# Kernel tuning notes

Hardware: AMD Instinct MI355X
Metric: run time of the kernel (lower is better)

Reference implementation:

```python
import jax, jax.numpy as jnp
import numpy as np

B, T, C = 16, 2048, 384
HEAD = 384

def setup_inputs() -> dict:
    key = jax.random.key(0)
    kx, kq, kk, kv = jax.random.split(key, 4)
    s = 1.0 / np.sqrt(C)
    return {
        "x": jax.random.normal(kx, (B, T, C), dtype=jnp.float32),
        "Wq": jax.random.normal(kq, (C, HEAD), dtype=jnp.float32) * s,
        "Wk": jax.random.normal(kk, (C, HEAD), dtype=jnp.float32) * s,
        "Wv": jax.random.normal(kv, (C, HEAD), dtype=jnp.float32) * s,
    }

def reference(x, Wq, Wk, Wv):
    # x: [B,T,C]; single causal attention head, eval mode (dropout = identity)
    Bc, Tc, Cc = x.shape
    q = jnp.einsum('btc,ch->bth', x, Wq)
    k = jnp.einsum('btc,ch->bth', x, Wk)
    v = jnp.einsum('btc,ch->bth', x, Wv)
    # NOTE: original scales by C**-0.5 (embedding dim), not head_size**-0.5
    scale = Cc ** (-0.5)
    wei = jnp.einsum('bth,bsh->bts', q, k) * scale  # [B,T,T]
    causal = jnp.tril(jnp.ones((Tc, Tc), dtype=bool))
    wei = jnp.where(causal, wei, -jnp.inf)
    wei = jax.nn.softmax(wei, axis=-1)
    out = jnp.einsum('bts,bsh->bth', wei, v)  # [B,T,head]
    return out
```

## Files before the change

### kernel.cpp

```cpp
#include <hip/hip_runtime.h>
#include <hip/hip_bf16.h>

#define NB 16
#define TT 2048
#define CC 384

typedef short bf16x8 __attribute__((ext_vector_type(8)));
typedef float f32x4 __attribute__((ext_vector_type(4)));

static __device__ __forceinline__ short f2bf(float f) {
  union { __hip_bfloat16 h; short s; } u;
  u.h = __float2bfloat16(f);
  return u.s;
}

#define QSC (0.051031036307982884f * 1.4426950408889634f)

__global__ __launch_bounds__(384)
void conv_wt(const float* __restrict__ Wq, const float* __restrict__ Wk,
             const float* __restrict__ Wv, short* __restrict__ Wbt) {
  const int w = blockIdx.x / CC;
  const int n = blockIdx.x % CC;
  const int k = threadIdx.x;
  const float* W = (w == 0) ? Wq : (w == 1) ? Wk : Wv;
  Wbt[((size_t)w * CC + n) * CC + k] = f2bf(W[(size_t)k * CC + n]);
}

__global__ __launch_bounds__(256, 3)
void proj_gemm(const float* __restrict__ x, const short* __restrict__ Wbt,
               short* __restrict__ Q, short* __restrict__ K,
               short* __restrict__ Vt) {
  __shared__ char smem[34816];
  short* As = (short*)smem;
  short* Bs = (short*)(smem + 10240);
  short* Es = (short*)smem;

  const int mt = blockIdx.x & 255;
  const int nt = blockIdx.x >> 8;
  const int wsel = nt / 3;
  const int nc0 = (nt % 3) * 128;
  const int tid = threadIdx.x;
  const int wave = tid >> 6, lane = tid & 63;
  const int l15 = lane & 15, quad = lane >> 4;
  const int wm = (wave & 1) * 64, wn = (wave >> 1) * 64;

  const float* Ab = x + (size_t)mt * 128 * CC;
  const short* Bb = Wbt + ((size_t)wsel * CC + nc0) * CC;

  f32x4 acc[16];
  #pragma unroll
  for (int i = 0; i < 16; ++i) acc[i] = f32x4{0.f, 0.f, 0.f, 0.f};

  float4 ra[4];
  bf16x8 rb[2];
  #pragma unroll
  for (int c = 0; c < 4; ++c) {
    const int ci = c * 256 + tid;
    ra[c] = *(const float4*)(Ab + (size_t)(ci >> 3) * CC + (ci & 7) * 4);
  }
  #pragma unroll
  for (int c = 0; c < 2; ++c) {
    const int ci = c * 256 + tid;
    rb[c] = *(const bf16x8*)(Bb + (size_t)(ci >> 2) * CC + (ci & 3) * 8);
  }

  for (int kt = 0; kt < 12; ++kt) {
    __syncthreads();
    #pragma unroll
    for (int c = 0; c < 4; ++c) {
      const int ci = c * 256 + tid;
      short4 s4;
      s4.x = f2bf(ra[c].x); s4.y = f2bf(ra[c].y);
      s4.z = f2bf(ra[c].z); s4.w = f2bf(ra[c].w);
      *(short4*)((char*)As + (ci >> 3) * 80 + (ci & 7) * 8) = s4;
    }
    #pragma unroll
    for (int c = 0; c < 2; ++c) {
      const int ci = c * 256 + tid;
      *(bf16x8*)((char*)Bs + (ci >> 2) * 80 + (ci & 3) * 16) = rb[c];
    }
    __syncthreads();
    if (kt < 11) {
      const int k0 = (kt + 1) * 32;
      #pragma unroll
      for (int c = 0; c < 4; ++c) {
        const int ci = c * 256 + tid;
        ra[c] = *(const float4*)(Ab + (size_t)(ci >> 3) * CC + k0 + (ci & 7) * 4);
      }
      #pragma unroll
      for (int c = 0; c < 2; ++c) {
        const int ci = c * 256 + tid;
        rb[c] = *(const bf16x8*)(Bb + (size_t)(ci >> 2) * CC + k0 + (ci & 3) * 8);
      }
    }
    bf16x8 af[4], bf[4];
    #pragma unroll
    for (int i = 0; i < 4; ++i) {
      af[i] = *(const bf16x8*)((char*)As + (wm + i * 16 + l15) * 80 + quad * 16);
      bf[i] = *(const bf16x8*)((char*)Bs + (wn + i * 16 + l15) * 80 + quad * 16);
    }
    #pragma unroll
    for (int i = 0; i < 4; ++i)
      #pragma unroll
      for (int j = 0; j < 4; ++j)
        acc[i * 4 + j] =
            __builtin_amdgcn_mfma_f32_16x16x32_bf16(af[i], bf[j], acc[i * 4 + j], 0, 0, 0);
  }

  if (nt < 6) {
    short* O = (nt < 3) ? Q : K;
    const float sc = (nt < 3) ? QSC : 1.0f;
    #pragma unroll
    for (int i = 0; i < 4; ++i)
      #pragma unroll
      for (int j = 0; j < 4; ++j) {
        const f32x4 a = acc[i * 4 + j];
        const int r0 = mt * 128 + wm + i * 16 + quad * 4;
        const int c = nc0 + wn + j * 16 + l15;
        #pragma unroll
        for (int r = 0; r < 4; ++r) O[(size_t)(r0 + r) * CC + c] = f2bf(a[r] * sc);
      }
  } else {
    __syncthreads();
    #pragma unroll
    for (int i = 0; i < 4; ++i)
      #pragma unroll
      for (int j = 0; j < 4; ++j) {
        const f32x4 a = acc[i * 4 + j];
        const int dl = wn + j * 16 + l15;
        const int ml = wm + i * 16 + quad * 4;
        short4 p4;
        p4.x = f2bf(a[0]); p4.y = f2bf(a[1]); p4.z = f2bf(a[2]); p4.w = f2bf(a[3]);
        *(short4*)(Es + (size_t)dl * 136 + ml) = p4;
      }
    __syncthreads();
    const int d0 = (nt - 6) * 128;
    const int b = mt >> 4, t0 = (mt & 15) * 128;
    const int dr = tid >> 1, hf = tid & 1;
    const short* src = Es + (size_t)dr * 136 + hf * 64;
    short* dst = Vt + ((size_t)b * CC + d0 + dr) * TT + t0 + hf * 64;
    #pragma unroll
    for (int c = 0; c < 8; ++c)
      *(bf16x8*)(dst + c * 8) = *(const bf16x8*)(src + c * 8);
  }
}

__global__ __launch_bounds__(256, 2)
void attn_kernel(const short* __restrict__ Q, const short* __restrict__ K,
                 const short* __restrict__ Vt, float* __restrict__ out) {
  __shared__ char sm[54272];
  char* Ks = sm;
  char* Vs = sm + 24576;
  short* Ps = (short*)(sm + 49152);

  const int blk = blockIdx.x;
  const int qt = 31 - (blk >> 4);
  const int b  = blk & 15;
  const int q0b = qt * 64;
  const int tid = threadIdx.x;
  const int wave = tid >> 6, lane = tid & 63;
  const int l15 = lane & 15, quad = lane >> 4;
  const int q0 = q0b + wave * 16;
  short* pw = Ps + wave * 640;

  bf16x8 qf[12];
  const short* qp = Q + ((size_t)b * TT + q0 + l15) * CC + quad * 8;
  #pragma unroll
  for (int ks = 0; ks < 12; ++ks) qf[ks] = *(const bf16x8*)(qp + ks * 32);

  f32x4 o[24];
  #pragma unroll
  for (int n = 0; n < 24; ++n) o[n] = f32x4{0.f, 0.f, 0.f, 0.f};
  f32x4 lsum = f32x4{0.f, 0.f, 0.f, 0.f};
  float m[4];
  #pragma unroll
  for (int r = 0; r < 4; ++r) m[r] = -INFINITY;

  bf16x8 onesf;
  #pragma unroll
  for (int i = 0; i < 8; ++i) onesf[i] = (short)0x3F80;

  int koff[6], voff[6];
  #pragma unroll
  for (int j = 0; j < 6; ++j) {
    const int lin = wave * 6144 + j * 1024 + lane * 16;
    const int kr = lin / 768;
    const int ksl = (lin - kr * 768) >> 4;
    koff[j] = kr * 768 + ((ksl ^ (kr & 7)) << 4);
    const int vr = lin >> 6;
    const int vsl = (lin >> 4) & 3;
    voff[j] = vr * 4096 + (((vsl - (vr >> 2)) & 3) << 4);
  }
  const char* kbB = (const char*)(K + (size_t)b * TT * CC);
  const char* vtB = (const char*)(Vt + (size_t)b * CC * TT);
  char* KsW = Ks + wave * 6144;
  char* VsW = Vs + wave * 6144;

  const int nchunk = qt * 2 + 2;

  #pragma unroll
  for (int j = 0; j < 6; ++j)
    __builtin_amdgcn_global_load_lds(
        (const __attribute__((address_space(1))) void*)(kbB + koff[j]),
        (__attribute__((address_space(3))) void*)(KsW + j * 1024), 16, 0, 0);
  #pragma unroll
  for (int j = 0; j < 6; ++j)
    __builtin_amdgcn_global_load_lds(
        (const __attribute__((address_space(1))) void*)(vtB + voff[j]),
        (__attribute__((address_space(3))) void*)(VsW + j * 1024), 16, 0, 0);

  for (int kc = 0; kc < nchunk; ++kc) {
    const int k0 = kc * 32;
    const bool active = (k0 <= q0 + 15);
    const int kn = (k0 + 32 < TT - 32) ? (k0 + 32) : (TT - 32);

    asm volatile("s_waitcnt vmcnt(6)" ::: "memory");
    __builtin_amdgcn_s_barrier();
    __builtin_amdgcn_sched_barrier(0);

    f32x4 s0 = f32x4{0.f, 0.f, 0.f, 0.f};
    f32x4 s1 = f32x4{0.f, 0.f, 0.f, 0.f};
    if (active) {
      #pragma unroll
      for (int ks = 0; ks < 12; ++ks) {
        const int sl = (ks * 4 + quad) ^ (l15 & 7);
        const bf16x8 b0 = *(const bf16x8*)(Ks + l15 * 768 + (sl << 4));
        const bf16x8 b1 = *(const bf16x8*)(Ks + (16 + l15) * 768 + (sl << 4));
        s0 = __builtin_amdgcn_mfma_f32_16x16x32_bf16(qf[ks], b0, s0, 0, 0, 0);
        s1 = __builtin_amdgcn_mfma_f32_16x16x32_bf16(qf[ks], b1, s1, 0, 0, 0);
      }
    }
    __builtin_amdgcn_sched_barrier(0);
    __builtin_amdgcn_s_barrier();

    #pragma unroll
    for (int j = 0; j < 6; ++j)
      __builtin_amdgcn_global_load_lds(
          (const __attribute__((address_space(1))) void*)(kbB + (size_t)kn * 768 + koff[j]),
          (__attribute__((address_space(3))) void*)(KsW + j * 1024), 16, 0, 0);

    asm volatile("s_waitcnt vmcnt(6)" ::: "memory");
    __builtin_amdgcn_s_barrier();
    __builtin_amdgcn_sched_barrier(0);

    if (active) {
      const bool domask = (k0 + 31 > q0);
      float mx[4];
      #pragma unroll
      for (int r = 0; r < 4; ++r) {
        float a = s0[r], c = s1[r];
        if (domask) {
          const int qg = q0 + quad * 4 + r;
          if (k0 + l15 > qg)      a = -INFINITY;
          if (k0 + 16 + l15 > qg) c = -INFINITY;
        }
        s0[r] = a; s1[r] = c;
        float v = fmaxf(a, c);
        v = fmaxf(v, __shfl_xor(v, 1));
        v = fmaxf(v, __shfl_xor(v, 2));
        v = fmaxf(v, __shfl_xor(v, 4));
        v = fmaxf(v, __shfl_xor(v, 8));
        mx[r] = v;
      }
      float alpha[4];
      #pragma unroll
      for (int r = 0; r < 4; ++r) {
        const float mn = fmaxf(m[r], mx[r]);
        alpha[r] = exp2f(m[r] - mn);
        m[r] = mn;
        s0[r] = exp2f(s0[r] - mn);
        s1[r] = exp2f(s1[r] - mn);
      }
      const bool need = (alpha[0] < 1.f) | (alpha[1] < 1.f) |
                        (alpha[2] < 1.f) | (alpha[3] < 1.f);
      if (__any(need)) {
        #pragma unroll
        for (int r = 0; r < 4; ++r) lsum[r] *= alpha[r];
        #pragma unroll
        for (int n = 0; n < 24; ++n) {
          #pragma unroll
          for (int r = 0; r < 4; ++r) o[n][r] *= alpha[r];
        }
      }
      #pragma unroll
      for (int r = 0; r < 4; ++r) {
        pw[(quad * 4 + r) * 40 + l15]      = f2bf(s0[r]);
        pw[(quad * 4 + r) * 40 + 16 + l15] = f2bf(s1[r]);
      }
      const bf16x8 pf = *(const bf16x8*)(pw + l15 * 40 + quad * 8);
      lsum = __builtin_amdgcn_mfma_f32_16x16x32_bf16(pf, onesf, lsum, 0, 0, 0);
      #pragma unroll
      for (int n = 0; n < 24; ++n) {
        const int vrow = n * 16 + l15;
        const bf16x8 vf = *(const bf16x8*)(Vs + vrow * 64 + (((quad + (vrow >> 2)) & 3) << 4));
        o[n] = __builtin_amdgcn_mfma_f32_16x16x32_bf16(pf, vf, o[n], 0, 0, 0);
      }
    }
    __builtin_amdgcn_sched_barrier(0);
    __builtin_amdgcn_s_barrier();
    #pragma unroll
    for (int j = 0; j < 6; ++j)
      __builtin_amdgcn_global_load_lds(
          (const __attribute__((address_space(1))) void*)(vtB + (size_t)kn * 2 + voff[j]),
          (__attribute__((address_space(3))) void*)(VsW + j * 1024), 16, 0, 0);
  }

  float linv[4];
  #pragma unroll
  for (int r = 0; r < 4; ++r) linv[r] = 1.f / lsum[r];
  float* ob = out + ((size_t)b * TT + q0) * CC;
  #pragma unroll
  for (int n = 0; n < 24; ++n) {
    #pragma unroll
    for (int r = 0; r < 4; ++r) {
      ob[(size_t)(quad * 4 + r) * CC + n * 16 + l15] = o[n][r] * linv[r];
    }
  }
}

extern "C" void kernel_launch(void* const* d_in, const int* in_sizes, int n_in,
                              void* d_out, int out_size, void* d_ws, size_t ws_size,
                              hipStream_t stream) {
  const float* x  = (const float*)d_in[0];
  const float* Wq = (const float*)d_in[1];
  const float* Wk = (const float*)d_in[2];
  const float* Wv = (const float*)d_in[3];
  float* out = (float*)d_out;

  const size_t QS = (size_t)NB * TT * CC;
  short* Qs = (short*)d_ws;
  short* Ks = Qs + QS;
  short* Vt = Ks + QS;

  short* Wbt = (short*)d_out;

  hipLaunchKernelGGL(conv_wt, dim3(3 * CC), dim3(CC), 0, stream, Wq, Wk, Wv, Wbt);
  hipLaunchKernelGGL(proj_gemm, dim3(256 * 9), dim3(256), 0, stream,
                     x, Wbt, Qs, Ks, Vt);
  hipLaunchKernelGGL(attn_kernel, dim3(NB * TT / 64), dim3(256), 0, stream,
                     Qs, Ks, Vt, out);
}
```

Measured before the change: 312.1 us.

## Pair causal query tiles per block and double-buffer K/V chunks in LDS

Each attention block now handles two query tiles, a long one (31-jj) and a short one (jj), so every block does the same amount of causal work. The grid is halved and occupancy drops to one block per CU. K and V chunks are now double-buffered in LDS, with both loaded two chunks ahead, replacing the single buffer whose K and V loads were interleaved with compute phases. The QK and PV phases merge into one active region with fewer barriers. The cost is double the LDS footprint and lower occupancy, which leaves less latency hiding from co-resident blocks.

Result: slower. 344.7 us (+10.5%).

```diff
diff --git a/kernel.cpp b/kernel.cpp
--- a/kernel.cpp
+++ b/kernel.cpp
@@ -145,36 +145,18 @@
   }
 }
 
-__global__ __launch_bounds__(256, 2)
+__global__ __launch_bounds__(256, 1)
 void attn_kernel(const short* __restrict__ Q, const short* __restrict__ K,
                  const short* __restrict__ Vt, float* __restrict__ out) {
-  __shared__ char sm[54272];
-  char* Ks = sm;
-  char* Vs = sm + 24576;
-  short* Ps = (short*)(sm + 49152);
+  __shared__ char sm[103424];
 
   const int blk = blockIdx.x;
-  const int qt = 31 - (blk >> 4);
+  const int jj = blk >> 4;
   const int b  = blk & 15;
-  const int q0b = qt * 64;
   const int tid = threadIdx.x;
   const int wave = tid >> 6, lane = tid & 63;
   const int l15 = lane & 15, quad = lane >> 4;
-  const int q0 = q0b + wave * 16;
-  short* pw = Ps + wave * 640;
-
-  bf16x8 qf[12];
-  const short* qp = Q + ((size_t)b * TT + q0 + l15) * CC + quad * 8;
-  #pragma unroll
-  for (int ks = 0; ks < 12; ++ks) qf[ks] = *(const bf16x8*)(qp + ks * 32);
-
-  f32x4 o[24];
-  #pragma unroll
-  for (int n = 0; n < 24; ++n) o[n] = f32x4{0.f, 0.f, 0.f, 0.f};
-  f32x4 lsum = f32x4{0.f, 0.f, 0.f, 0.f};
-  float m[4];
-  #pragma unroll
-  for (int r = 0; r < 4; ++r) m[r] = -INFINITY;
+  short* pw = (short*)(sm + 98304) + wave * 640;
 
   bf16x8 onesf;
   #pragma unroll
@@ -193,127 +175,152 @@
   }
   const char* kbB = (const char*)(K + (size_t)b * TT * CC);
   const char* vtB = (const char*)(Vt + (size_t)b * CC * TT);
-  char* KsW = Ks + wave * 6144;
-  char* VsW = Vs + wave * 6144;
-
-  const int nchunk = qt * 2 + 2;
-
-  #pragma unroll
-  for (int j = 0; j < 6; ++j)
-    __builtin_amdgcn_global_load_lds(
-        (const __attribute__((address_space(1))) void*)(kbB + koff[j]),
-        (__attribute__((address_space(3))) void*)(KsW + j * 1024), 16, 0, 0);
-  #pragma unroll
-  for (int j = 0; j < 6; ++j)
-    __builtin_amdgcn_global_load_lds(
-        (const __attribute__((address_space(1))) void*)(vtB + voff[j]),
-        (__attribute__((address_space(3))) void*)(VsW + j * 1024), 16, 0, 0);
-
-  for (int kc = 0; kc < nchunk; ++kc) {
-    const int k0 = kc * 32;
-    const bool active = (k0 <= q0 + 15);
-    const int kn = (k0 + 32 < TT - 32) ? (k0 + 32) : (TT - 32);
-
-    asm volatile("s_waitcnt vmcnt(6)" ::: "memory");
-    __builtin_amdgcn_s_barrier();
-    __builtin_amdgcn_sched_barrier(0);
-
-    f32x4 s0 = f32x4{0.f, 0.f, 0.f, 0.f};
-    f32x4 s1 = f32x4{0.f, 0.f, 0.f, 0.f};
-    if (active) {
-      #pragma unroll
-      for (int ks = 0; ks < 12; ++ks) {
-        const int sl = (ks * 4 + quad) ^ (l15 & 7);
-        const bf16x8 b0 = *(const bf16x8*)(Ks + l15 * 768 + (sl << 4));
-        const bf16x8 b1 = *(const bf16x8*)(Ks + (16 + l15) * 768 + (sl << 4));
-        s0 = __builtin_amdgcn_mfma_f32_16x16x32_bf16(qf[ks], b0, s0, 0, 0, 0);
-        s1 = __builtin_amdgcn_mfma_f32_16x16x32_bf16(qf[ks], b1, s1, 0, 0, 0);
-      }
-    }
-    __builtin_amdgcn_sched_barrier(0);
-    __builtin_amdgcn_s_barrier();
-
-    #pragma unroll
-    for (int j = 0; j < 6; ++j)
-      __builtin_amdgcn_global_load_lds(
-          (const __attribute__((address_space(1))) void*)(kbB + (size_t)kn * 768 + koff[j]),
-          (__attribute__((address_space(3))) void*)(KsW + j * 1024), 16, 0, 0);
-
-    asm volatile("s_waitcnt vmcnt(6)" ::: "memory");
-    __builtin_amdgcn_s_barrier();
-    __builtin_amdgcn_sched_barrier(0);
-
-    if (active) {
-      const bool domask = (k0 + 31 > q0);
-      float mx[4];
+
+  #pragma unroll 1
+  for (int half = 0; half < 2; ++half) {
+    const int qt = half ? jj : (31 - jj);
+    const int q0 = qt * 64 + wave * 16;
+    const int nchunk = qt * 2 + 2;
+
+    bf16x8 qf[12];
+    const short* qp = Q + ((size_t)b * TT + q0 + l15) * CC + quad * 8;
+    #pragma unroll
+    for (int ks = 0; ks < 12; ++ks) qf[ks] = *(const bf16x8*)(qp + ks * 32);
+    asm volatile("s_waitcnt vmcnt(0)" ::: "memory");
+
+    f32x4 o[24];
+    #pragma unroll
+    for (int n = 0; n < 24; ++n) o[n] = f32x4{0.f, 0.f, 0.f, 0.f};
+    f32x4 lsum = f32x4{0.f, 0.f, 0.f, 0.f};
+    float m[4];
+    #pragma unroll
+    for (int r = 0; r < 4; ++r) m[r] = -INFINITY;
+
+    #pragma unroll
+    for (int pc = 0; pc < 2; ++pc) {
+      char* KsW = sm + pc * 24576 + wave * 6144;
+      char* VsW = sm + 49152 + pc * 24576 + wave * 6144;
+      const size_t kby = (size_t)pc * 24576;
+      const size_t vby = (size_t)pc * 64;
+      #pragma unroll
+      for (int j = 0; j < 6; ++j)
+        __builtin_amdgcn_global_load_lds(
+            (const __attribute__((address_space(1))) void*)(kbB + kby + koff[j]),
+            (__attribute__((address_space(3))) void*)(KsW + j * 1024), 16, 0, 0);
+      #pragma unroll
+      for (int j = 0; j < 6; ++j)
+        __builtin_amdgcn_global_load_lds(
+            (const __attribute__((address_space(1))) void*)(vtB + vby + voff[j]),
+            (__attribute__((address_space(3))) void*)(VsW + j * 1024), 16, 0, 0);
+    }
+
+    for (int kc = 0; kc < nchunk; ++kc) {
+      const int k0 = kc * 32;
+      const int kb = kc & 1;
+      if (kc + 1 == nchunk) {
+        asm volatile("s_waitcnt vmcnt(0)" ::: "memory");
+      } else {
+        asm volatile("s_waitcnt vmcnt(12)" ::: "memory");
+      }
+      __builtin_amdgcn_s_barrier();
+      __builtin_amdgcn_sched_barrier(0);
+
+      const bool active = (k0 <= q0 + 15);
+      if (active) {
+        const char* Ksb = sm + kb * 24576;
+        const char* Vsb = sm + 49152 + kb * 24576;
+        f32x4 s0 = f32x4{0.f, 0.f, 0.f, 0.f};
+        f32x4 s1 = f32x4{0.f, 0.f, 0.f, 0.f};
+        #pragma unroll
+        for (int ks = 0; ks < 12; ++ks) {
+          const int sl = (ks * 4 + quad) ^ (l15 & 7);
+          const bf16x8 b0 = *(const bf16x8*)(Ksb + l15 * 768 + (sl << 4));
+          const bf16x8 b1 = *(const bf16x8*)(Ksb + (16 + l15) * 768 + (sl << 4));
+          s0 = __builtin_amdgcn_mfma_f32_16x16x32_bf16(qf[ks], b0, s0, 0, 0, 0);
+          s1 = __builtin_amdgcn_mfma_f32_16x16x32_bf16(qf[ks], b1, s1, 0, 0, 0);
+        }
+        const bool domask = (k0 + 31 > q0);
+        float mx[4];
+        #pragma unroll
+        for (int r = 0; r < 4; ++r) {
+          float a = s0[r], c = s1[r];
+          if (domask) {
+            const int qg = q0 + quad * 4 + r;
+            if (k0 + l15 > qg)      a = -INFINITY;
+            if (k0 + 16 + l15 > qg) c = -INFINITY;
+          }
+          s0[r] = a; s1[r] = c;
+          float v = fmaxf(a, c);
+          v = fmaxf(v, __shfl_xor(v, 1));
+          v = fmaxf(v, __shfl_xor(v, 2));
+          v = fmaxf(v, __shfl_xor(v, 4));
+          v = fmaxf(v, __shfl_xor(v, 8));
+          mx[r] = v;
+        }
+        float alpha[4];
+        #pragma unroll
+        for (int r = 0; r < 4; ++r) {
+          const float mn = fmaxf(m[r], mx[r]);
+          alpha[r] = exp2f(m[r] - mn);
+          m[r] = mn;
+          s0[r] = exp2f(s0[r] - mn);
+          s1[r] = exp2f(s1[r] - mn);
+        }
+        const bool need = (alpha[0] < 1.f) | (alpha[1] < 1.f) |
+                          (alpha[2] < 1.f) | (alpha[3] < 1.f);
+        if (__any(need)) {
+          #pragma unroll
+          for (int r = 0; r < 4; ++r) lsum[r] *= alpha[r];
+          #pragma unroll
+          for (int n = 0; n < 24; ++n) {
+            #pragma unroll
+            for (int r = 0; r < 4; ++r) o[n][r] *= alpha[r];
+          }
+        }
+        #pragma unroll
+        for (int r = 0; r < 4; ++r) {
+          pw[(quad * 4 + r) * 40 + l15]      = f2bf(s0[r]);
+          pw[(quad * 4 + r) * 40 + 16 + l15] = f2bf(s1[r]);
+        }
+        const bf16x8 pf = *(const bf16x8*)(pw + l15 * 40 + quad * 8);
+        lsum = __builtin_amdgcn_mfma_f32_16x16x32_bf16(pf, onesf, lsum, 0, 0, 0);
+        #pragma unroll
+        for (int n = 0; n < 24; ++n) {
+          const int vrow = n * 16 + l15;
+          const bf16x8 vf = *(const bf16x8*)(Vsb + vrow * 64 + (((quad + (vrow >> 2)) & 3) << 4));
+          o[n] = __builtin_amdgcn_mfma_f32_16x16x32_bf16(pf, vf, o[n], 0, 0, 0);
+        }
+      }
+      __builtin_amdgcn_sched_barrier(0);
+      __builtin_amdgcn_s_barrier();
+      if (kc + 2 < nchunk) {
+        char* KsW = sm + kb * 24576 + wave * 6144;
+        char* VsW = sm + 49152 + kb * 24576 + wave * 6144;
+        const size_t kby = (size_t)(kc + 2) * 24576;
+        const size_t vby = (size_t)(kc + 2) * 64;
+        #pragma unroll
+        for (int j = 0; j < 6; ++j)
+          __builtin_amdgcn_global_load_lds(
+              (const __attribute__((address_space(1))) void*)(kbB + kby + koff[j]),
+              (__attribute__((address_space(3))) void*)(KsW + j * 1024), 16, 0, 0);
+        #pragma unroll
+        for (int j = 0; j < 6; ++j)
+          __builtin_amdgcn_global_load_lds(
+              (const __attribute__((address_space(1))) void*)(vtB + vby + voff[j]),
+              (__attribute__((address_space(3))) void*)(VsW + j * 1024), 16, 0, 0);
+      }
+    }
+
+    float linv[4];
+    #pragma unroll
+    for (int r = 0; r < 4; ++r) linv[r] = 1.f / lsum[r];
+    float* ob = out + ((size_t)b * TT + q0) * CC;
+    #pragma unroll
+    for (int n = 0; n < 24; ++n) {
       #pragma unroll
       for (int r = 0; r < 4; ++r) {
-        float a = s0[r], c = s1[r];
-        if (domask) {
-          const int qg = q0 + quad * 4 + r;
-          if (k0 + l15 > qg)      a = -INFINITY;
-          if (k0 + 16 + l15 > qg) c = -INFINITY;
-        }
-        s0[r] = a; s1[r] = c;
-        float v = fmaxf(a, c);
-        v = fmaxf(v, __shfl_xor(v, 1));
-        v = fmaxf(v, __shfl_xor(v, 2));
-        v = fmaxf(v, __shfl_xor(v, 4));
-        v = fmaxf(v, __shfl_xor(v, 8));
-        mx[r] = v;
-      }
-      float alpha[4];
-      #pragma unroll
-      for (int r = 0; r < 4; ++r) {
-        const float mn = fmaxf(m[r], mx[r]);
-        alpha[r] = exp2f(m[r] - mn);
-        m[r] = mn;
-        s0[r] = exp2f(s0[r] - mn);
-        s1[r] = exp2f(s1[r] - mn);
-      }
-      const bool need = (alpha[0] < 1.f) | (alpha[1] < 1.f) |
-                        (alpha[2] < 1.f) | (alpha[3] < 1.f);
-      if (__any(need)) {
-        #pragma unroll
-        for (int r = 0; r < 4; ++r) lsum[r] *= alpha[r];
-        #pragma unroll
-        for (int n = 0; n < 24; ++n) {
-          #pragma unroll
-          for (int r = 0; r < 4; ++r) o[n][r] *= alpha[r];
-        }
-      }
-      #pragma unroll
-      for (int r = 0; r < 4; ++r) {
-        pw[(quad * 4 + r) * 40 + l15]      = f2bf(s0[r]);
-        pw[(quad * 4 + r) * 40 + 16 + l15] = f2bf(s1[r]);
-      }
-      const bf16x8 pf = *(const bf16x8*)(pw + l15 * 40 + quad * 8);
-      lsum = __builtin_amdgcn_mfma_f32_16x16x32_bf16(pf, onesf, lsum, 0, 0, 0);
-      #pragma unroll
-      for (int n = 0; n < 24; ++n) {
-        const int vrow = n * 16 + l15;
-        const bf16x8 vf = *(const bf16x8*)(Vs + vrow * 64 + (((quad + (vrow >> 2)) & 3) << 4));
-        o[n] = __builtin_amdgcn_mfma_f32_16x16x32_bf16(pf, vf, o[n], 0, 0, 0);
-      }
-    }
-    __builtin_amdgcn_sched_barrier(0);
-    __builtin_amdgcn_s_barrier();
-    #pragma unroll
-    for (int j = 0; j < 6; ++j)
-      __builtin_amdgcn_global_load_lds(
-          (const __attribute__((address_space(1))) void*)(vtB + (size_t)kn * 2 + voff[j]),
-          (__attribute__((address_space(3))) void*)(VsW + j * 1024), 16, 0, 0);
-  }
-
-  float linv[4];
-  #pragma unroll
-  for (int r = 0; r < 4; ++r) linv[r] = 1.f / lsum[r];
-  float* ob = out + ((size_t)b * TT + q0) * CC;
-  #pragma unroll
-  for (int n = 0; n < 24; ++n) {
-    #pragma unroll
-    for (int r = 0; r < 4; ++r) {
-      ob[(size_t)(quad * 4 + r) * CC + n * 16 + l15] = o[n][r] * linv[r];
+        ob[(size_t)(quad * 4 + r) * CC + n * 16 + l15] = o[n][r] * linv[r];
+      }
     }
   }
 }
@@ -337,6 +344,6 @@
   hipLaunchKernelGGL(conv_wt, dim3(3 * CC), dim3(CC), 0, stream, Wq, Wk, Wv, Wbt);
   hipLaunchKernelGGL(proj_gemm, dim3(256 * 9), dim3(256), 0, stream,
                      x, Wbt, Qs, Ks, Vt);
-  hipLaunchKernelGGL(attn_kernel, dim3(NB * TT / 64), dim3(256), 0, stream,
+  hipLaunchKernelGGL(attn_kernel, dim3(NB * TT / 128), dim3(256), 0, stream,
                      Qs, Ks, Vt, out);
 }
```
